# Performance work log

Hardware: AMD Instinct MI355X
Metric: run time of the kernel (lower is better)

## Reference

```python
import jax, jax.numpy as jnp
import numpy as np

N, IN_DIM, OUT_DIM, BATCH = 8192, 128, 128, 4


def _glorot(key, shape):
    lim = float(np.sqrt(6.0 / (shape[0] + shape[1])))
    return jax.random.uniform(key, shape, jnp.float32, -lim, lim)


def setup_inputs() -> dict:
    key = jax.random.key(0)
    ks = jax.random.split(key, 16)
    inp = {
        "x": jax.random.normal(ks[0], (BATCH, N, IN_DIM), jnp.float32),
        "L0": jax.random.normal(ks[1], (N, N), jnp.float32) / np.sqrt(N),
        "L1": jax.random.normal(ks[2], (N, N), jnp.float32) / np.sqrt(N),
        "L2": jax.random.normal(ks[3], (N, N), jnp.float32) / np.sqrt(N),
        "L3": jax.random.normal(ks[4], (N, N), jnp.float32) / np.sqrt(N),
    }
    # 8 GCN layers: (branch b, layer l) -> W_bl, bias_bl
    kidx = 5
    for b in range(4):
        for l in range(2):
            d_in = IN_DIM if l == 0 else OUT_DIM
            inp[f"W{b}{l}"] = _glorot(ks[kidx], (d_in, OUT_DIM))
            inp[f"b{b}{l}"] = jnp.zeros((OUT_DIM,), jnp.float32)
            kidx += 1
    return inp


def _gcn_block(L, x, W, b):
    # support = L @ x  (graph propagation), then dense transform + ReLU
    support = jnp.einsum("nm,bmf->bnf", L, x)  # [B, N, F_in]
    return jax.nn.relu(support @ W + b)        # [B, N, F_out]


def reference(x, L0, L1, L2, L3,
              W00, b00, W01, b01,
              W10, b10, W11, b11,
              W20, b20, W21, b21,
              W30, b30, W31, b31):
    x0 = _gcn_block(L0, _gcn_block(L0, x, W00, b00), W01, b01)
    x1 = _gcn_block(L1, _gcn_block(L1, x, W10, b10), W11, b11)
    x2 = _gcn_block(L2, _gcn_block(L2, x, W20, b20), W21, b21)
    x3 = _gcn_block(L3, _gcn_block(L3, x, W30, b30), W31, b31)
    return (x0, x1, x2, x3)
```

## Files before the change

kernel.cpp:

```cpp
#include <hip/hip_runtime.h>
#include <stdint.h>


typedef short bf16x8 __attribute__((ext_vector_type(8)));
typedef float f32x4  __attribute__((ext_vector_type(4)));
typedef float f32x16 __attribute__((ext_vector_type(16)));

static __device__ __forceinline__ unsigned short f2bf(float f) {
  __bf16 h = (__bf16)f;
  return __builtin_bit_cast(unsigned short, h);
}
static __device__ __forceinline__ unsigned int pack2(float a, float b) {
  return (unsigned int)f2bf(a) | ((unsigned int)f2bf(b) << 16);
}
static __device__ __forceinline__ bf16x8 cvt8(float4 lo, float4 hi) {
  bf16x8 r;
  r[0] = (short)f2bf(lo.x); r[1] = (short)f2bf(lo.y);
  r[2] = (short)f2bf(lo.z); r[3] = (short)f2bf(lo.w);
  r[4] = (short)f2bf(hi.x); r[5] = (short)f2bf(hi.y);
  r[6] = (short)f2bf(hi.z); r[7] = (short)f2bf(hi.w);
  return r;
}

#define GLOAD16(g, l)                                                                  \
  __builtin_amdgcn_global_load_lds((const __attribute__((address_space(1))) void*)(g), \
                                   (__attribute__((address_space(3))) void*)(l), 16, 0, 0)

struct WPtrs { const float* w[8]; };
__global__ __launch_bounds__(256)
void prep_w(WPtrs p, unsigned short* __restrict__ wt) {
  const int s = blockIdx.x;
  const float* W = p.w[s];
  unsigned short* dst = wt + s * 16384;
  for (int i = threadIdx.x; i < 16384; i += 256) {
    const int fi = i >> 7, fo = i & 127;
    dst[fo * 128 + fi] = f2bf(W[i]);
  }
}

template <int AFP32>
__global__ __launch_bounds__(256)
void small_gemm(const float* __restrict__ x, const unsigned short* __restrict__ H1m,
                const unsigned short* __restrict__ WT, unsigned short* __restrict__ Z) {
  __shared__ unsigned short Sa[128 * 136];

  const int t = threadIdx.x, lane = t & 63, wave = t >> 6;
  const int l15 = lane & 15, lk = (lane >> 4) * 8;
  const int wm = (wave >> 1) * 64, wn = (wave & 1) * 64;
  const int mt = blockIdx.x, br = blockIdx.y;
  const int batch = mt >> 6, node0 = (mt & 63) * 128;

  {
    const int row = t >> 1, seg = (t & 1) * 64;
    if (AFP32) {
      const float4* src = (const float4*)(x + ((size_t)batch * 8192 + node0 + row) * 128 + seg);
      uint4* dst = (uint4*)&Sa[row * 136 + seg];
#pragma unroll
      for (int i = 0; i < 8; ++i) {
        float4 a = src[i * 2], b = src[i * 2 + 1];
        uint4 v;
        v.x = pack2(a.x, a.y); v.y = pack2(a.z, a.w);
        v.z = pack2(b.x, b.y); v.w = pack2(b.z, b.w);
        dst[i] = v;
      }
    } else {
      const uint4* src = (const uint4*)(H1m + ((size_t)(br * 4 + batch) * 8192 + node0 + row) * 128 + seg);
      uint4* dst = (uint4*)&Sa[row * 136 + seg];
#pragma unroll
      for (int i = 0; i < 8; ++i) dst[i] = src[i];
    }
  }
  __syncthreads();

  const unsigned short* WTb = WT + (size_t)(2 * br + (AFP32 ? 0 : 1)) * 16384;
  f32x4 acc[4][4];
#pragma unroll
  for (int i = 0; i < 4; ++i)
#pragma unroll
    for (int j = 0; j < 4; ++j) acc[i][j] = f32x4{0.f, 0.f, 0.f, 0.f};

#pragma unroll
  for (int kk = 0; kk < 4; ++kk) {
    bf16x8 av[4], wv[4];
#pragma unroll
    for (int mi = 0; mi < 4; ++mi)
      av[mi] = *(const bf16x8*)&Sa[(wm + mi * 16 + l15) * 136 + kk * 32 + lk];
#pragma unroll
    for (int ni = 0; ni < 4; ++ni)
      wv[ni] = *(const bf16x8*)&WTb[(wn + ni * 16 + l15) * 128 + kk * 32 + lk];
#pragma unroll
    for (int mi = 0; mi < 4; ++mi)
#pragma unroll
      for (int ni = 0; ni < 4; ++ni)
        acc[mi][ni] = __builtin_amdgcn_mfma_f32_16x16x32_bf16(av[mi], wv[ni], acc[mi][ni], 0, 0, 0);
  }

#pragma unroll
  for (int mi = 0; mi < 4; ++mi) {
#pragma unroll
    for (int ni = 0; ni < 4; ++ni) {
      const int row0 = wm + mi * 16 + (lane >> 4) * 4;
      const int col  = wn + ni * 16 + l15;
      uint2 pv;
      pv.x = pack2(acc[mi][ni][0], acc[mi][ni][1]);
      pv.y = pack2(acc[mi][ni][2], acc[mi][ni][3]);
      *(uint2*)(Z + ((size_t)br * 512 + batch * 128 + col) * 8192 + node0 + row0) = pv;
    }
  }
}

struct BigArgs {
  const float* L[4];
  const float* bias[4];
  const unsigned short* Z;
  void* Dst;
};

template <int LAYER>
__global__ __launch_bounds__(512, 2)
void big_gemm(BigArgs a) {
  extern __shared__ char smem[];

  const int t = threadIdx.x, lane = t & 63, wave = t >> 6;
  const int l31 = lane & 31, hk = lane >> 5;
  const int wm = (wave >> 2) * 128, wn = (wave & 3) * 64;

  const int bid = blockIdx.x;
  const int work = (bid & 7) * 32 + (bid >> 3);
  const int nb = work & 1, mt = (work >> 1) & 31, br = work >> 6;
  const int mbase = mt * 256;

  const float* A = a.L[br];
  const float* bias = a.bias[br];
  const unsigned short* Zb = a.Z + (size_t)br * (512 * 8192);

  const int arow = t >> 1, ah = t & 1;
  const float* aG = A + (size_t)(mbase + arow) * 8192 + ah * 16;
  const int c0 = 2 * ah, akey = (arow >> 1) & 3;
  char* aRowL = smem + arow * 64;
  const unsigned short* bG = Zb + (size_t)(nb * 256 + wave * 32 + (lane >> 2)) * 8192
                                + ((lane & 3) ^ ((lane >> 3) & 3)) * 8;
  char* bWave = smem + 32768 + wave * 2048;

  const int aBase = (wm + l31) * 64;
  const int bBase = (wn + l31) * 64;
  const int key4 = (l31 >> 1) & 3;

  f32x16 c00{}, c01{}, c10{}, c11{}, c20{}, c21{}, c30{}, c31{};
  float4 s0[4], s1[4], s2[4];
  bf16x8 av0, av1, av2, av3, bv0, bv1;

#define GLB(T_) do {                                                   \
    const unsigned short* _bp = bG + (size_t)(T_) * 32;                \
    char* _bl = bWave + ((T_) & 3) * 16384;                            \
    GLOAD16(_bp, _bl);                                                 \
    GLOAD16(_bp + 16 * 8192, _bl + 1024); } while (0)

#define LOADA(T_, R) do {                                              \
    const float* _ap = aG + (size_t)(T_) * 32;                         \
    R[0] = *(const float4*)(_ap);                                      \
    R[1] = *(const float4*)(_ap + 4);                                  \
    R[2] = *(const float4*)(_ap + 8);                                  \
    R[3] = *(const float4*)(_ap + 12); } while (0)

#define WRITEA(T_, R) do {                                             \
    char* _al = aRowL + (((T_) & 1)) * 16384;                          \
    *(bf16x8*)(_al + ((c0 ^ akey) * 16))       = cvt8(R[0], R[1]);     \
    *(bf16x8*)(_al + (((c0 + 1) ^ akey) * 16)) = cvt8(R[2], R[3]); } while (0)

#define RD(ab_, bb_, s_) do {                                          \
    const int _ch = ((2 * (s_) + hk) ^ key4) * 16;                     \
    av0 = *(const bf16x8*)((ab_) + aBase + _ch);                       \
    av1 = *(const bf16x8*)((ab_) + aBase + 2048 + _ch);                \
    av2 = *(const bf16x8*)((ab_) + aBase + 4096 + _ch);                \
    av3 = *(const bf16x8*)((ab_) + aBase + 6144 + _ch);                \
    bv0 = *(const bf16x8*)((bb_) + bBase + _ch);                       \
    bv1 = *(const bf16x8*)((bb_) + bBase + 2048 + _ch); } while (0)

#define DO_MFMA() do {                                                       \
    __builtin_amdgcn_s_setprio(1);                                           \
    c00 = __builtin_amdgcn_mfma_f32_32x32x16_bf16(av0, bv0, c00, 0, 0, 0);   \
    c01 = __builtin_amdgcn_mfma_f32_32x32x16_bf16(av0, bv1, c01, 0, 0, 0);   \
    c10 = __builtin_amdgcn_mfma_f32_32x32x16_bf16(av1, bv0, c10, 0, 0, 0);   \
    c11 = __builtin_amdgcn_mfma_f32_32x32x16_bf16(av1, bv1, c11, 0, 0, 0);   \
    c20 = __builtin_amdgcn_mfma_f32_32x32x16_bf16(av2, bv0, c20, 0, 0, 0);   \
    c21 = __builtin_amdgcn_mfma_f32_32x32x16_bf16(av2, bv1, c21, 0, 0, 0);   \
    c30 = __builtin_amdgcn_mfma_f32_32x32x16_bf16(av3, bv0, c30, 0, 0, 0);   \
    c31 = __builtin_amdgcn_mfma_f32_32x32x16_bf16(av3, bv1, c31, 0, 0, 0);   \
    __builtin_amdgcn_s_setprio(0); } while (0)

#define ITER(T_, SLOAD, SWRITE, VMSTR, DO_STAGE, DO_WRITE) do {        \
    asm volatile("s_waitcnt " VMSTR ::: "memory");                     \
    asm volatile("s_waitcnt lgkmcnt(0)" ::: "memory");                 \
    __builtin_amdgcn_s_barrier();                                      \
    if (DO_STAGE) { GLB((T_) + 3); LOADA((T_) + 3, SLOAD); }           \
    const char* _ab = smem + ((T_) & 1) * 16384;                       \
    const char* _bb = smem + 32768 + ((T_) & 3) * 16384;               \
    RD(_ab, _bb, 0);                                                   \
    DO_MFMA();                                                         \
    if (DO_WRITE) WRITEA((T_) + 1, SWRITE);                            \
    RD(_ab, _bb, 1);                                                   \
    DO_MFMA();                                                         \
  } while (0)

  GLB(0); LOADA(0, s0);
  GLB(1); LOADA(1, s1);
  GLB(2); LOADA(2, s2);
  WRITEA(0, s0);

  for (int T = 0; T < 252; T += 3) {
    ITER(T,     s0, s1, "vmcnt(12)", 1, 1);
    ITER(T + 1, s1, s2, "vmcnt(12)", 1, 1);
    ITER(T + 2, s2, s0, "vmcnt(12)", 1, 1);
  }
  ITER(252, s0, s1, "vmcnt(12)", 1, 1);
  ITER(253, s0, s2, "vmcnt(12)", 0, 1);
  ITER(254, s0, s0, "vmcnt(6)",  0, 1);
  ITER(255, s0, s0, "vmcnt(0)",  0, 0);

#undef ITER
#undef DO_MFMA
#undef RD
#undef WRITEA
#undef LOADA
#undef GLB

  __syncthreads();

  if (LAYER == 0) {
    unsigned short* S16 = (unsigned short*)smem;
#define EPI16(AM, BN, ACC) do {                                             \
    const int col = (wave & 1) * 64 + (BN) * 32 + l31;                      \
    const float bvv = bias[col];                                            \
    _Pragma("unroll") for (int r = 0; r < 16; ++r) {                        \
      const int row = wm + (AM) * 32 + (r & 3) + 8 * (r >> 2) + 4 * hk;     \
      S16[row * 136 + col] = f2bf(fmaxf(ACC[r] + bvv, 0.f));                \
    } } while (0)
#pragma unroll
    for (int h = 0; h < 2; ++h) {
      if (((wave >> 1) & 1) == h) {
        EPI16(0, 0, c00); EPI16(0, 1, c01);
        EPI16(1, 0, c10); EPI16(1, 1, c11);
        EPI16(2, 0, c20); EPI16(2, 1, c21);
        EPI16(3, 0, c30); EPI16(3, 1, c31);
      }
      __syncthreads();
      const int batch = nb * 2 + h;
      const int row = t >> 1, seg = (t & 1) * 64;
      unsigned short* Dst = (unsigned short*)a.Dst;
      const uint4* src = (const uint4*)&S16[row * 136 + seg];
      uint4* dst = (uint4*)(Dst + ((size_t)(br * 4 + batch) * 8192 + mbase + row) * 128 + seg);
#pragma unroll
      for (int i = 0; i < 8; ++i) dst[i] = src[i];
      __syncthreads();
    }
#undef EPI16
  } else {
    float* S32 = (float*)smem;
#define EPI32(AM, BN, ACC) do {                                             \
    const int col = (wave & 1) * 64 + (BN) * 32 + l31;                      \
    const float bvv = bias[col];                                            \
    _Pragma("unroll") for (int r = 0; r < 16; ++r) {                        \
      const int lrow = (AM) * 32 + (r & 3) + 8 * (r >> 2) + 4 * hk;         \
      S32[lrow * 128 + col] = fmaxf(ACC[r] + bvv, 0.f);                     \
    } } while (0)
#pragma unroll
    for (int h = 0; h < 2; ++h) {
#pragma unroll
      for (int rh = 0; rh < 2; ++rh) {
        if (((wave >> 1) & 1) == h && (wave >> 2) == rh) {
          EPI32(0, 0, c00); EPI32(0, 1, c01);
          EPI32(1, 0, c10); EPI32(1, 1, c11);
          EPI32(2, 0, c20); EPI32(2, 1, c21);
          EPI32(3, 0, c30); EPI32(3, 1, c31);
        }
        __syncthreads();
        const int batch = nb * 2 + h;
        const int row = t >> 2, seg = (t & 3) * 32;
        float* Dst = (float*)a.Dst;
        const float4* src = (const float4*)&S32[row * 128 + seg];
        float4* dst = (float4*)(Dst + ((size_t)(br * 4 + batch) * 8192 + mbase + rh * 128 + row) * 128 + seg);
#pragma unroll
        for (int i = 0; i < 8; ++i) dst[i] = src[i];
        __syncthreads();
      }
    }
#undef EPI32
  }
}

extern "C" void kernel_launch(void* const* d_in, const int* in_sizes, int n_in,
                              void* d_out, int out_size, void* d_ws, size_t ws_size,
                              hipStream_t stream) {
  const float* x = (const float*)d_in[0];
  unsigned short* Z   = (unsigned short*)d_ws;
  unsigned short* H1m = Z + (size_t)4 * 512 * 8192;
  unsigned short* WT  = H1m + (size_t)4 * 4 * 8192 * 128;
  float* out = (float*)d_out;

  static int attr_done = 0;
  if (!attr_done) {
    hipFuncSetAttribute((const void*)big_gemm<0>, hipFuncAttributeMaxDynamicSharedMemorySize, 98304);
    hipFuncSetAttribute((const void*)big_gemm<1>, hipFuncAttributeMaxDynamicSharedMemorySize, 98304);
    attr_done = 1;
  }

  WPtrs wp;
  for (int b = 0; b < 4; ++b) {
    wp.w[b * 2 + 0] = (const float*)d_in[5 + b * 4 + 0];
    wp.w[b * 2 + 1] = (const float*)d_in[5 + b * 4 + 2];
  }
  prep_w<<<8, 256, 0, stream>>>(wp, WT);

  BigArgs a0, a1;
  for (int b = 0; b < 4; ++b) {
    a0.L[b] = (const float*)d_in[1 + b];
    a1.L[b] = (const float*)d_in[1 + b];
    a0.bias[b] = (const float*)d_in[6 + b * 4];
    a1.bias[b] = (const float*)d_in[8 + b * 4];
  }
  a0.Z = Z; a0.Dst = (void*)H1m;
  a1.Z = Z; a1.Dst = (void*)out;

  small_gemm<1><<<dim3(256, 4), 256, 0, stream>>>(x, nullptr, WT, Z);
  big_gemm<0><<<256, 512, 98304, stream>>>(a0);
  small_gemm<0><<<dim3(256, 4), 256, 0, stream>>>(nullptr, H1m, WT, Z);
  big_gemm<1><<<256, 512, 98304, stream>>>(a1);
}
```

Baseline: 1.008 ms.

## Pre-convert Laplacians to tiled bf16 once and stream tiles via direct LDS loads

Adds a conv_l kernel that converts the four fp32 Laplacians each call into a pre-swizzled, tile-major bf16 buffer in workspace. Both big GEMM layers then load A tiles with global_load_lds, using a 4-stage ring buffer and 128KB of LDS. This drops the per-iteration register load, fp32→bf16 conversion and LDS writes of A, and halves A bytes in the GEMMs. The cost is an extra conversion pass that writes 512MB of workspace, and likely lower occupancy because the launch-bounds occupancy hint was removed. The old path stays as a fallback when the workspace is too small.

```diff
diff --git a/kernel.cpp b/kernel.cpp
--- a/kernel.cpp
+++ b/kernel.cpp
@@ -36,6 +36,35 @@
     const int fi = i >> 7, fo = i & 127;
     dst[fo * 128 + fi] = f2bf(W[i]);
   }
+}
+
+struct LPtrs { const float* l[4]; };
+__global__ __launch_bounds__(256)
+void conv_l(LPtrs p, char* __restrict__ lbf) {
+  __shared__ char T[65536];
+  const int t = threadIdx.x, lane = t & 63, wave = t >> 6;
+  const int rg = blockIdx.x, kg = blockIdx.y, br = blockIdx.z;
+  const float* L = p.l[br];
+  const int r0 = rg * 64, k0 = kg * 512;
+  const int mt = rg >> 2, rowoff = (rg & 3) * 64, kt0 = kg * 16;
+#pragma unroll
+  for (int i = 0; i < 16; ++i) {
+    const int rr = wave * 16 + i;
+    const float* src = L + (size_t)(r0 + rr) * 8192 + k0;
+#pragma unroll
+    for (int half = 0; half < 2; ++half) {
+      float4 v = ((const float4*)src)[half * 64 + lane];
+      const int ktl = half * 8 + (lane >> 3);
+      const int ch  = ((lane >> 1) & 3) ^ ((rr >> 1) & 3);
+      uint2 pv; pv.x = pack2(v.x, v.y); pv.y = pack2(v.z, v.w);
+      *(uint2*)(T + ktl * 4096 + rr * 64 + ch * 16 + (lane & 1) * 8) = pv;
+    }
+  }
+  __syncthreads();
+  char* dstb = lbf + ((size_t)(br * 32 + mt) * 256 + kt0) * 16384 + rowoff * 64;
+#pragma unroll
+  for (int ktl = 0; ktl < 16; ++ktl)
+    ((uint4*)(dstb + (size_t)ktl * 16384))[t] = ((const uint4*)(T + ktl * 4096))[t];
 }
 
 template <int AFP32>
@@ -115,67 +144,6 @@
   const unsigned short* Z;
   void* Dst;
 };
-
-template <int LAYER>
-__global__ __launch_bounds__(512, 2)
-void big_gemm(BigArgs a) {
-  extern __shared__ char smem[];
-
-  const int t = threadIdx.x, lane = t & 63, wave = t >> 6;
-  const int l31 = lane & 31, hk = lane >> 5;
-  const int wm = (wave >> 2) * 128, wn = (wave & 3) * 64;
-
-  const int bid = blockIdx.x;
-  const int work = (bid & 7) * 32 + (bid >> 3);
-  const int nb = work & 1, mt = (work >> 1) & 31, br = work >> 6;
-  const int mbase = mt * 256;
-
-  const float* A = a.L[br];
-  const float* bias = a.bias[br];
-  const unsigned short* Zb = a.Z + (size_t)br * (512 * 8192);
-
-  const int arow = t >> 1, ah = t & 1;
-  const float* aG = A + (size_t)(mbase + arow) * 8192 + ah * 16;
-  const int c0 = 2 * ah, akey = (arow >> 1) & 3;
-  char* aRowL = smem + arow * 64;
-  const unsigned short* bG = Zb + (size_t)(nb * 256 + wave * 32 + (lane >> 2)) * 8192
-                                + ((lane & 3) ^ ((lane >> 3) & 3)) * 8;
-  char* bWave = smem + 32768 + wave * 2048;
-
-  const int aBase = (wm + l31) * 64;
-  const int bBase = (wn + l31) * 64;
-  const int key4 = (l31 >> 1) & 3;
-
-  f32x16 c00{}, c01{}, c10{}, c11{}, c20{}, c21{}, c30{}, c31{};
-  float4 s0[4], s1[4], s2[4];
-  bf16x8 av0, av1, av2, av3, bv0, bv1;
-
-#define GLB(T_) do {                                                   \
-    const unsigned short* _bp = bG + (size_t)(T_) * 32;                \
-    char* _bl = bWave + ((T_) & 3) * 16384;                            \
-    GLOAD16(_bp, _bl);                                                 \
-    GLOAD16(_bp + 16 * 8192, _bl + 1024); } while (0)
-
-#define LOADA(T_, R) do {                                              \
-    const float* _ap = aG + (size_t)(T_) * 32;                         \
-    R[0] = *(const float4*)(_ap);                                      \
-    R[1] = *(const float4*)(_ap + 4);                                  \
-    R[2] = *(const float4*)(_ap + 8);                                  \
-    R[3] = *(const float4*)(_ap + 12); } while (0)
-
-#define WRITEA(T_, R) do {                                             \
-    char* _al = aRowL + (((T_) & 1)) * 16384;                          \
-    *(bf16x8*)(_al + ((c0 ^ akey) * 16))       = cvt8(R[0], R[1]);     \
-    *(bf16x8*)(_al + (((c0 + 1) ^ akey) * 16)) = cvt8(R[2], R[3]); } while (0)
-
-#define RD(ab_, bb_, s_) do {                                          \
-    const int _ch = ((2 * (s_) + hk) ^ key4) * 16;                     \
-    av0 = *(const bf16x8*)((ab_) + aBase + _ch);                       \
-    av1 = *(const bf16x8*)((ab_) + aBase + 2048 + _ch);                \
-    av2 = *(const bf16x8*)((ab_) + aBase + 4096 + _ch);                \
-    av3 = *(const bf16x8*)((ab_) + aBase + 6144 + _ch);                \
-    bv0 = *(const bf16x8*)((bb_) + bBase + _ch);                       \
-    bv1 = *(const bf16x8*)((bb_) + bBase + 2048 + _ch); } while (0)
 
 #define DO_MFMA() do {                                                       \
     __builtin_amdgcn_s_setprio(1);                                           \
@@ -189,6 +157,192 @@
     c31 = __builtin_amdgcn_mfma_f32_32x32x16_bf16(av3, bv1, c31, 0, 0, 0);   \
     __builtin_amdgcn_s_setprio(0); } while (0)
 
+#define RD(ab_, bb_, s_) do {                                          \
+    const int _ch = ((2 * (s_) + hk) ^ key4) * 16;                     \
+    av0 = *(const bf16x8*)((ab_) + aBase + _ch);                       \
+    av1 = *(const bf16x8*)((ab_) + aBase + 2048 + _ch);                \
+    av2 = *(const bf16x8*)((ab_) + aBase + 4096 + _ch);                \
+    av3 = *(const bf16x8*)((ab_) + aBase + 6144 + _ch);                \
+    bv0 = *(const bf16x8*)((bb_) + bBase + _ch);                       \
+    bv1 = *(const bf16x8*)((bb_) + bBase + 2048 + _ch); } while (0)
+
+#define BIG_EPILOGUE()                                                                     \
+  __syncthreads();                                                                          \
+  if (LAYER == 0) {                                                                         \
+    unsigned short* S16 = (unsigned short*)smem;                                            \
+    _Pragma("unroll")                                                                       \
+    for (int h = 0; h < 2; ++h) {                                                           \
+      if (((wave >> 1) & 1) == h) {                                                         \
+        EPI16(0, 0, c00); EPI16(0, 1, c01);                                                 \
+        EPI16(1, 0, c10); EPI16(1, 1, c11);                                                 \
+        EPI16(2, 0, c20); EPI16(2, 1, c21);                                                 \
+        EPI16(3, 0, c30); EPI16(3, 1, c31);                                                 \
+      }                                                                                     \
+      __syncthreads();                                                                      \
+      const int batch = nb * 2 + h;                                                         \
+      const int row = t >> 1, seg = (t & 1) * 64;                                           \
+      unsigned short* Dst = (unsigned short*)a.Dst;                                         \
+      const uint4* src = (const uint4*)&S16[row * 136 + seg];                               \
+      uint4* dst = (uint4*)(Dst + ((size_t)(br * 4 + batch) * 8192 + mbase + row) * 128 + seg); \
+      _Pragma("unroll") for (int i = 0; i < 8; ++i) dst[i] = src[i];                        \
+      __syncthreads();                                                                      \
+    }                                                                                       \
+  } else {                                                                                  \
+    float* S32 = (float*)smem;                                                              \
+    _Pragma("unroll")                                                                       \
+    for (int h = 0; h < 2; ++h) {                                                           \
+      _Pragma("unroll")                                                                     \
+      for (int rh = 0; rh < 2; ++rh) {                                                      \
+        if (((wave >> 1) & 1) == h && (wave >> 2) == rh) {                                  \
+          EPI32(0, 0, c00); EPI32(0, 1, c01);                                               \
+          EPI32(1, 0, c10); EPI32(1, 1, c11);                                               \
+          EPI32(2, 0, c20); EPI32(2, 1, c21);                                               \
+          EPI32(3, 0, c30); EPI32(3, 1, c31);                                               \
+        }                                                                                   \
+        __syncthreads();                                                                    \
+        const int batch = nb * 2 + h;                                                       \
+        const int row = t >> 2, seg = (t & 3) * 32;                                         \
+        float* Dst = (float*)a.Dst;                                                         \
+        const float4* src = (const float4*)&S32[row * 128 + seg];                           \
+        float4* dst = (float4*)(Dst + ((size_t)(br * 4 + batch) * 8192 + mbase + rh * 128 + row) * 128 + seg); \
+        _Pragma("unroll") for (int i = 0; i < 8; ++i) dst[i] = src[i];                      \
+        __syncthreads();                                                                    \
+      }                                                                                     \
+    }                                                                                       \
+  }
+
+#define EPI16(AM, BN, ACC) do {                                             \
+    const int col = (wave & 1) * 64 + (BN) * 32 + l31;                      \
+    const float bvv = bias[col];                                            \
+    _Pragma("unroll") for (int r = 0; r < 16; ++r) {                        \
+      const int row = wm + (AM) * 32 + (r & 3) + 8 * (r >> 2) + 4 * hk;     \
+      S16[row * 136 + col] = f2bf(fmaxf(ACC[r] + bvv, 0.f));                \
+    } } while (0)
+#define EPI32(AM, BN, ACC) do {                                             \
+    const int col = (wave & 1) * 64 + (BN) * 32 + l31;                      \
+    const float bvv = bias[col];                                            \
+    _Pragma("unroll") for (int r = 0; r < 16; ++r) {                        \
+      const int lrow = (AM) * 32 + (r & 3) + 8 * (r >> 2) + 4 * hk;         \
+      S32[lrow * 128 + col] = fmaxf(ACC[r] + bvv, 0.f);                     \
+    } } while (0)
+
+template <int LAYER>
+__global__ __launch_bounds__(512)
+void big_gemm_pc(BigArgs a, const char* __restrict__ Lbf) {
+  extern __shared__ char smem[];
+
+  const int t = threadIdx.x, lane = t & 63, wave = t >> 6;
+  const int l31 = lane & 31, hk = lane >> 5;
+  const int wm = (wave >> 2) * 128, wn = (wave & 3) * 64;
+
+  const int bid = blockIdx.x;
+  const int work = (bid & 7) * 32 + (bid >> 3);
+  const int nb = work & 1, mt = (work >> 1) & 31, br = work >> 6;
+  const int mbase = mt * 256;
+
+  const float* bias = a.bias[br];
+  const unsigned short* Zb = a.Z + (size_t)br * (512 * 8192);
+
+  const char* aTiles = Lbf + ((size_t)(br * 32 + mt) * 256) * 16384;
+  const unsigned short* bG = Zb + (size_t)(nb * 256 + wave * 32 + (lane >> 2)) * 8192
+                                + ((lane & 3) ^ ((lane >> 3) & 3)) * 8;
+
+  const int aBase = (wm + l31) * 64;
+  const int bBase = (wn + l31) * 64;
+  const int key4 = (l31 >> 1) & 3;
+
+  f32x16 c00{}, c01{}, c10{}, c11{}, c20{}, c21{}, c30{}, c31{};
+  bf16x8 av0, av1, av2, av3, bv0, bv1;
+
+#define STG(T_) do {                                                          \
+    const char* _as = aTiles + (size_t)(T_) * 16384 + wave * 2048 + lane * 16;\
+    char* _ad = smem + ((T_) & 3) * 16384 + wave * 2048;                      \
+    GLOAD16(_as, _ad);                                                        \
+    GLOAD16(_as + 1024, _ad + 1024);                                          \
+    const unsigned short* _bp = bG + (size_t)(T_) * 32;                       \
+    char* _bl = smem + 65536 + ((T_) & 3) * 16384 + wave * 2048;              \
+    GLOAD16(_bp, _bl);                                                        \
+    GLOAD16(_bp + 16 * 8192, _bl + 1024); } while (0)
+
+#define ITER(T_, VMSTR, DO_STG) do {                                          \
+    asm volatile("s_waitcnt " VMSTR ::: "memory");                            \
+    __builtin_amdgcn_s_barrier();                                             \
+    if (DO_STG) STG((T_) + 3);                                                \
+    const char* _ab = smem + ((T_) & 3) * 16384;                              \
+    const char* _bb = smem + 65536 + ((T_) & 3) * 16384;                      \
+    RD(_ab, _bb, 0);                                                          \
+    DO_MFMA();                                                                \
+    RD(_ab, _bb, 1);                                                          \
+    DO_MFMA();                                                                \
+  } while (0)
+
+  STG(0); STG(1); STG(2);
+
+  for (int T = 0; T < 252; T += 4) {
+    ITER(T,     "vmcnt(8)", 1);
+    ITER(T + 1, "vmcnt(8)", 1);
+    ITER(T + 2, "vmcnt(8)", 1);
+    ITER(T + 3, "vmcnt(8)", 1);
+  }
+  ITER(252, "vmcnt(8)", 1);
+  ITER(253, "vmcnt(8)", 0);
+  ITER(254, "vmcnt(4)", 0);
+  ITER(255, "vmcnt(0)", 0);
+#undef ITER
+#undef STG
+
+  BIG_EPILOGUE()
+}
+
+template <int LAYER>
+__global__ __launch_bounds__(512, 2)
+void big_gemm_rs(BigArgs a) {
+  extern __shared__ char smem[];
+
+  const int t = threadIdx.x, lane = t & 63, wave = t >> 6;
+  const int l31 = lane & 31, hk = lane >> 5;
+  const int wm = (wave >> 2) * 128, wn = (wave & 3) * 64;
+
+  const int bid = blockIdx.x;
+  const int work = (bid & 7) * 32 + (bid >> 3);
+  const int nb = work & 1, mt = (work >> 1) & 31, br = work >> 6;
+  const int mbase = mt * 256;
+
+  const float* A = a.L[br];
+  const float* bias = a.bias[br];
+  const unsigned short* Zb = a.Z + (size_t)br * (512 * 8192);
+
+  const int arow = t >> 1, ah = t & 1;
+  const float* aG = A + (size_t)(mbase + arow) * 8192 + ah * 16;
+  const int c0 = 2 * ah, akey = (arow >> 1) & 3;
+  char* aRowL = smem + arow * 64;
+  const unsigned short* bG = Zb + (size_t)(nb * 256 + wave * 32 + (lane >> 2)) * 8192
+                                + ((lane & 3) ^ ((lane >> 3) & 3)) * 8;
+  char* bWave = smem + 32768 + wave * 2048;
+
+  const int aBase = (wm + l31) * 64;
+  const int bBase = (wn + l31) * 64;
+  const int key4 = (l31 >> 1) & 3;
+
+  f32x16 c00{}, c01{}, c10{}, c11{}, c20{}, c21{}, c30{}, c31{};
+  float4 s0[4], s1[4], s2[4];
+  bf16x8 av0, av1, av2, av3, bv0, bv1;
+
+#define GLB(T_) do {                                                   \
+    const unsigned short* _bp = bG + (size_t)(T_) * 32;                \
+    char* _bl = bWave + ((T_) & 3) * 16384;                            \
+    GLOAD16(_bp, _bl);                                                 \
+    GLOAD16(_bp + 16 * 8192, _bl + 1024); } while (0)
+#define LOADA(T_, R) do {                                              \
+    const float* _ap = aG + (size_t)(T_) * 32;                         \
+    R[0] = *(const float4*)(_ap);                                      \
+    R[1] = *(const float4*)(_ap + 4);                                  \
+    R[2] = *(const float4*)(_ap + 8);                                  \
+    R[3] = *(const float4*)(_ap + 12); } while (0)
+#define WRITEA(T_, R) do {                                             \
+    char* _al = aRowL + (((T_) & 1)) * 16384;                          \
+    *(bf16x8*)(_al + ((c0 ^ akey) * 16))       = cvt8(R[0], R[1]);     \
+    *(bf16x8*)(_al + (((c0 + 1) ^ akey) * 16)) = cvt8(R[2], R[3]); } while (0)
 #define ITER(T_, SLOAD, SWRITE, VMSTR, DO_STAGE, DO_WRITE) do {        \
     asm volatile("s_waitcnt " VMSTR ::: "memory");                     \
     asm volatile("s_waitcnt lgkmcnt(0)" ::: "memory");                 \
@@ -217,76 +371,12 @@
   ITER(253, s0, s2, "vmcnt(12)", 0, 1);
   ITER(254, s0, s0, "vmcnt(6)",  0, 1);
   ITER(255, s0, s0, "vmcnt(0)",  0, 0);
-
 #undef ITER
-#undef DO_MFMA
-#undef RD
 #undef WRITEA
 #undef LOADA
 #undef GLB
 
-  __syncthreads();
-
-  if (LAYER == 0) {
-    unsigned short* S16 = (unsigned short*)smem;
-#define EPI16(AM, BN, ACC) do {                                             \
-    const int col = (wave & 1) * 64 + (BN) * 32 + l31;                      \
-    const float bvv = bias[col];                                            \
-    _Pragma("unroll") for (int r = 0; r < 16; ++r) {                        \
-      const int row = wm + (AM) * 32 + (r & 3) + 8 * (r >> 2) + 4 * hk;     \
-      S16[row * 136 + col] = f2bf(fmaxf(ACC[r] + bvv, 0.f));                \
-    } } while (0)
-#pragma unroll
-    for (int h = 0; h < 2; ++h) {
-      if (((wave >> 1) & 1) == h) {
-        EPI16(0, 0, c00); EPI16(0, 1, c01);
-        EPI16(1, 0, c10); EPI16(1, 1, c11);
-        EPI16(2, 0, c20); EPI16(2, 1, c21);
-        EPI16(3, 0, c30); EPI16(3, 1, c31);
-      }
-      __syncthreads();
-      const int batch = nb * 2 + h;
-      const int row = t >> 1, seg = (t & 1) * 64;
-      unsigned short* Dst = (unsigned short*)a.Dst;
-      const uint4* src = (const uint4*)&S16[row * 136 + seg];
-      uint4* dst = (uint4*)(Dst + ((size_t)(br * 4 + batch) * 8192 + mbase + row) * 128 + seg);
-#pragma unroll
-      for (int i = 0; i < 8; ++i) dst[i] = src[i];
-      __syncthreads();
-    }
-#undef EPI16
-  } else {
-    float* S32 = (float*)smem;
-#define EPI32(AM, BN, ACC) do {                                             \
-    const int col = (wave & 1) * 64 + (BN) * 32 + l31;                      \
-    const float bvv = bias[col];                                            \
-    _Pragma("unroll") for (int r = 0; r < 16; ++r) {                        \
-      const int lrow = (AM) * 32 + (r & 3) + 8 * (r >> 2) + 4 * hk;         \
-      S32[lrow * 128 + col] = fmaxf(ACC[r] + bvv, 0.f);                     \
-    } } while (0)
-#pragma unroll
-    for (int h = 0; h < 2; ++h) {
-#pragma unroll
-      for (int rh = 0; rh < 2; ++rh) {
-        if (((wave >> 1) & 1) == h && (wave >> 2) == rh) {
-          EPI32(0, 0, c00); EPI32(0, 1, c01);
-          EPI32(1, 0, c10); EPI32(1, 1, c11);
-          EPI32(2, 0, c20); EPI32(2, 1, c21);
-          EPI32(3, 0, c30); EPI32(3, 1, c31);
-        }
-        __syncthreads();
-        const int batch = nb * 2 + h;
-        const int row = t >> 2, seg = (t & 3) * 32;
-        float* Dst = (float*)a.Dst;
-        const float4* src = (const float4*)&S32[row * 128 + seg];
-        float4* dst = (float4*)(Dst + ((size_t)(br * 4 + batch) * 8192 + mbase + rh * 128 + row) * 128 + seg);
-#pragma unroll
-        for (int i = 0; i < 8; ++i) dst[i] = src[i];
-        __syncthreads();
-      }
-    }
-#undef EPI32
-  }
+  BIG_EPILOGUE()
 }
 
 extern "C" void kernel_launch(void* const* d_in, const int* in_sizes, int n_in,
@@ -296,12 +386,18 @@
   unsigned short* Z   = (unsigned short*)d_ws;
   unsigned short* H1m = Z + (size_t)4 * 512 * 8192;
   unsigned short* WT  = H1m + (size_t)4 * 4 * 8192 * 128;
+  char* Lbf = (char*)(WT + 8 * 16384);
   float* out = (float*)d_out;
+
+  const size_t NEED_PC = (size_t)33554432 + 33554432 + 262144 + 536870912;
+  const bool use_pc = ws_size >= NEED_PC;
 
   static int attr_done = 0;
   if (!attr_done) {
-    hipFuncSetAttribute((const void*)big_gemm<0>, hipFuncAttributeMaxDynamicSharedMemorySize, 98304);
-    hipFuncSetAttribute((const void*)big_gemm<1>, hipFuncAttributeMaxDynamicSharedMemorySize, 98304);
+    hipFuncSetAttribute((const void*)big_gemm_pc<0>, hipFuncAttributeMaxDynamicSharedMemorySize, 131072);
+    hipFuncSetAttribute((const void*)big_gemm_pc<1>, hipFuncAttributeMaxDynamicSharedMemorySize, 131072);
+    hipFuncSetAttribute((const void*)big_gemm_rs<0>, hipFuncAttributeMaxDynamicSharedMemorySize, 98304);
+    hipFuncSetAttribute((const void*)big_gemm_rs<1>, hipFuncAttributeMaxDynamicSharedMemorySize, 98304);
     attr_done = 1;
   }
 
@@ -322,8 +418,18 @@
   a0.Z = Z; a0.Dst = (void*)H1m;
   a1.Z = Z; a1.Dst = (void*)out;
 
-  small_gemm<1><<<dim3(256, 4), 256, 0, stream>>>(x, nullptr, WT, Z);
-  big_gemm<0><<<256, 512, 98304, stream>>>(a0);
-  small_gemm<0><<<dim3(256, 4), 256, 0, stream>>>(nullptr, H1m, WT, Z);
-  big_gemm<1><<<256, 512, 98304, stream>>>(a1);
-}
+  if (use_pc) {
+    LPtrs lp;
+    for (int b = 0; b < 4; ++b) lp.l[b] = (const float*)d_in[1 + b];
+    conv_l<<<dim3(128, 16, 4), 256, 0, stream>>>(lp, Lbf);
+    small_gemm<1><<<dim3(256, 4), 256, 0, stream>>>(x, nullptr, WT, Z);
+    big_gemm_pc<0><<<256, 512, 131072, stream>>>(a0, Lbf);
+    small_gemm<0><<<dim3(256, 4), 256, 0, stream>>>(nullptr, H1m, WT, Z);
+    big_gemm_pc<1><<<256, 512, 131072, stream>>>(a1, Lbf);
+  } else {
+    small_gemm<1><<<dim3(256, 4), 256, 0, stream>>>(x, nullptr, WT, Z);
+    big_gemm_rs<0><<<256, 512, 98304, stream>>>(a0);
+    small_gemm<0><<<dim3(256, 4), 256, 0, stream>>>(nullptr, H1m, WT, Z);
+    big_gemm_rs<1><<<256, 512, 98304, stream>>>(a1);
+  }
+}
```

Measured after the change: 934.8 us. 7.3% less time.
